# Kernel tuning notes

Measured on AMD Instinct MI355X. Metric: run time of the kernel, lower is better.

The kernel has to match this reference:

```python
import jax, jax.numpy as jnp
import numpy as np
import math

B, T, F_ = 4, 1024, 1024
TO_DIM, FROM_DIM, LATENT, H = 1024, 1024, 1024, 16
HEAD_DIM = LATENT // H

def _linear_params(key, in_dim, out_dim):
    kw, kb = jax.random.split(key)
    bound = 1.0 / math.sqrt(in_dim)
    W = jax.random.uniform(kw, (out_dim, in_dim), minval=-bound, maxval=bound, dtype=jnp.float32)
    b = jax.random.uniform(kb, (out_dim,), minval=-bound, maxval=bound, dtype=jnp.float32)
    return W, b

def setup_inputs() -> dict:
    key = jax.random.key(0)
    ks = jax.random.split(key, 7)
    X_to = jax.random.normal(ks[0], (B, T, TO_DIM), dtype=jnp.float32)
    X_from = jax.random.normal(ks[1], (B, F_, FROM_DIM), dtype=jnp.float32)
    mask_from = jax.random.randint(ks[2], (B, T, F_), 0, 2, dtype=jnp.int32)
    Wq, bq = _linear_params(ks[3], TO_DIM, LATENT)
    Wk, bk = _linear_params(ks[4], FROM_DIM, LATENT)
    Wv, bv = _linear_params(ks[5], FROM_DIM, LATENT)
    Wo, bo = _linear_params(ks[6], LATENT, TO_DIM)
    return {"X_to": X_to, "X_from": X_from, "mask_from": mask_from,
            "Wq": Wq, "bq": bq, "Wk": Wk, "bk": bk, "Wv": Wv, "bv": bv, "Wo": Wo, "bo": bo}

def _split_heads(x):
    # [b, t, (h k)] -> [b, h, t, k]
    b, t, _ = x.shape
    return x.reshape(b, t, H, HEAD_DIM).transpose(0, 2, 1, 3)

def reference(X_to, X_from, mask_from, Wq, bq, Wk, bk, Wv, bv, Wo, bo):
    Q = _split_heads(X_to @ Wq.T + bq)
    # NOTE: source swaps names — K comes from v_linear, V from k_linear. Reproduced literally.
    K = _split_heads(X_from @ Wv.T + bv)
    V = _split_heads(X_from @ Wk.T + bk)
    attn = jnp.einsum('bhtk,bhfk->bhtf', Q, K) / math.sqrt(HEAD_DIM)
    attn = jnp.where(mask_from[:, None, :, :] == 0, jnp.float32(-10000.0), attn)
    attn = jax.nn.softmax(attn, axis=-1)
    out = jnp.einsum('bhtf,bhfk->bhtk', attn, V)  # [b,h,t,k]
    out = out.transpose(0, 2, 1, 3).reshape(X_to.shape[0], X_to.shape[1], LATENT)
    return out @ Wo.T + bo
```

## Files before the change

### kernel.cpp

```cpp
#include <hip/hip_runtime.h>
#include <hip/hip_bf16.h>
#include <math.h>

#define BB 4
#define TT 1024
#define FF 1024
#define DIM 1024
#define NH 16
#define HD 64
#define MROWS (BB * TT)
#define FB (FF / 64)

typedef __attribute__((ext_vector_type(8))) short short8;
typedef __attribute__((ext_vector_type(4))) short short4v;
typedef __attribute__((ext_vector_type(4))) float f32x4;
typedef __hip_bfloat16 bf16;

__device__ __forceinline__ void async_copy16(const void* g, void* l) {
    __builtin_amdgcn_global_load_lds((const __attribute__((address_space(1))) void*)g,
                                     (__attribute__((address_space(3))) void*)l,
                                     16, 0, 0);
}

struct ConvArgs {
    const float* src[6];
    bf16* dst[6];
    int nvec[6];
    int blk_end[6];
    const int* mask;
    unsigned long long* Mb;
};

__global__ __launch_bounds__(256) void convert_pack(ConvArgs a) {
    int bx = blockIdx.x;
    if (bx >= a.blk_end[5]) {
        const int lane = threadIdx.x & 63;
        const int waveId = (bx - a.blk_end[5]) * 4 + (threadIdx.x >> 6);
#pragma unroll
        for (int it = 0; it < 16; ++it) {
            int c = waveId * 16 + it;
            int v = a.mask[(size_t)c * 64 + lane];
            unsigned long long bits = __ballot(v != 0);
            if (lane == 0) a.Mb[c] = bits;
        }
        return;
    }
    int seg = 0;
#pragma unroll
    for (int k = 0; k < 5; ++k) if (bx >= a.blk_end[k]) seg = k + 1;
    int b0 = seg ? a.blk_end[seg - 1] : 0;
    int idx = (bx - b0) * 256 + threadIdx.x;
    if (idx >= a.nvec[seg]) return;
    float4 v = ((const float4*)a.src[seg])[idx];
    union { bf16 t[4]; ushort4 u; } o;
    o.t[0] = __float2bfloat16(v.x);
    o.t[1] = __float2bfloat16(v.y);
    o.t[2] = __float2bfloat16(v.z);
    o.t[3] = __float2bfloat16(v.w);
    *(ushort4*)(a.dst[seg] + 4 * (size_t)idx) = o.u;
}

#define BK 64

struct QkvArgs {
    const bf16* A[3]; const bf16* W[3]; const float* bias[3]; bf16* C[3];
    int N[3]; int biasRow[3];
};

__global__ __launch_bounds__(256) void gemm_qkv(QkvArgs q) {
    __shared__ bf16 smem[128 * 132];
    bf16* As = smem;
    bf16* Bs = smem + 128 * BK;

    const int op = blockIdx.z;
    const bf16* A = q.A[op];
    const bf16* W = q.W[op];
    const float* bias = q.bias[op];
    bf16* C = q.C[op];
    const int N = q.N[op];
    const int brow = q.biasRow[op];

    const int lin = blockIdx.x + 8 * blockIdx.y;
    const int xcd = lin & 7;
    const int t   = lin >> 3;
    int m0, n0;
    if (brow) {
        m0 = (((t & 7) + xcd) & 7) * 128;
        n0 = (xcd * 4 + (t >> 3)) * 128;
    } else {
        m0 = (xcd * 4 + (t >> 3)) * 128;
        n0 = (((t & 7) + xcd) & 7) * 128;
    }

    const int tid  = threadIdx.x;
    const int lane = tid & 63;
    const int wave = tid >> 6;
    const int quad = lane >> 4;
    const int l16  = lane & 15;
    const int wm = wave & 1;
    const int wn = wave >> 1;
    const int wbase = tid & ~63;

    f32x4 acc[4][4] = {};

    for (int k0 = 0; k0 < DIM; k0 += BK) {
#pragma unroll
        for (int j = 0; j < 4; ++j) {
            int slot = j * 256 + tid;
            int r = slot >> 3;
            int g = (slot & 7) ^ (r & 7);
            async_copy16(A + (size_t)(m0 + r) * DIM + k0 + g * 8,
                         As + (size_t)(j * 256 + wbase) * 8);
            async_copy16(W + (size_t)(n0 + r) * DIM + k0 + g * 8,
                         Bs + (size_t)(j * 256 + wbase) * 8);
        }
        __syncthreads();

#pragma unroll
        for (int kk = 0; kk < 2; ++kk) {
            short8 a[4], b[4];
#pragma unroll
            for (int mi = 0; mi < 4; ++mi) {
                int r = wm * 64 + mi * 16 + l16;
                int p = (kk * 4 + quad) ^ (r & 7);
                a[mi] = *(const short8*)(As + r * BK + p * 8);
            }
#pragma unroll
            for (int ni = 0; ni < 4; ++ni) {
                int r = wn * 64 + ni * 16 + l16;
                int p = (kk * 4 + quad) ^ (r & 7);
                b[ni] = *(const short8*)(Bs + r * BK + p * 8);
            }
#pragma unroll
            for (int mi = 0; mi < 4; ++mi)
#pragma unroll
                for (int ni = 0; ni < 4; ++ni)
                    acc[mi][ni] = __builtin_amdgcn_mfma_f32_16x16x32_bf16(
                        a[mi], b[ni], acc[mi][ni], 0, 0, 0);
        }
        __syncthreads();
    }

    bf16* Cs = smem;
#pragma unroll
    for (int ni = 0; ni < 4; ++ni) {
        const int nl = wn * 64 + ni * 16 + l16;
        float bcol = brow ? 0.0f : bias[n0 + nl];
#pragma unroll
        for (int mi = 0; mi < 4; ++mi)
#pragma unroll
            for (int i = 0; i < 4; ++i) {
                const int ml = wm * 64 + mi * 16 + quad * 4 + i;
                float v = acc[mi][ni][i] + (brow ? bias[m0 + ml] : bcol);
                Cs[ml * 132 + nl] = __float2bfloat16(v);
            }
    }
    __syncthreads();
#pragma unroll
    for (int j = 0; j < 8; ++j) {
        int slot = j * 256 + tid;
        int rr = slot >> 4, cc = slot & 15;
        short8 v = *(const short8*)(Cs + rr * 132 + cc * 8);
        *(short8*)(C + (size_t)(m0 + rr) * N + n0 + cc * 8) = v;
    }
}

__global__ __launch_bounds__(256) void gemm_o(
    const bf16* __restrict__ A, const bf16* __restrict__ W,
    const float* __restrict__ bias, float* __restrict__ C)
{
    __shared__ float smemf[128 * 66];
    bf16* As = (bf16*)smemf;
    bf16* Bs = As + 128 * BK;

    const int lin = blockIdx.x + 16 * blockIdx.y;
    const int xcd = lin & 7;
    const int t   = lin >> 3;
    const int m0 = (xcd * 4 + (t >> 4)) * 128;
    const int n0 = (((t & 15) + 2 * xcd) & 15) * 64;

    const int tid  = threadIdx.x;
    const int lane = tid & 63;
    const int wave = tid >> 6;
    const int quad = lane >> 4;
    const int l16  = lane & 15;
    const int wm = wave & 1;
    const int wn = wave >> 1;
    const int wbase = tid & ~63;

    f32x4 acc[4][2] = {};

    for (int k0 = 0; k0 < DIM; k0 += BK) {
#pragma unroll
        for (int j = 0; j < 4; ++j) {
            int slot = j * 256 + tid;
            int r = slot >> 3;
            int g = (slot & 7) ^ (r & 7);
            async_copy16(A + (size_t)(m0 + r) * DIM + k0 + g * 8,
                         As + (size_t)(j * 256 + wbase) * 8);
        }
#pragma unroll
        for (int j = 0; j < 2; ++j) {
            int slot = j * 256 + tid;
            int r = slot >> 3;
            int g = (slot & 7) ^ (r & 7);
            async_copy16(W + (size_t)(n0 + r) * DIM + k0 + g * 8,
                         Bs + (size_t)(j * 256 + wbase) * 8);
        }
        __syncthreads();

#pragma unroll
        for (int kk = 0; kk < 2; ++kk) {
            short8 a[4], b[2];
#pragma unroll
            for (int mi = 0; mi < 4; ++mi) {
                int r = wm * 64 + mi * 16 + l16;
                int p = (kk * 4 + quad) ^ (r & 7);
                a[mi] = *(const short8*)(As + r * BK + p * 8);
            }
#pragma unroll
            for (int ni = 0; ni < 2; ++ni) {
                int r = wn * 32 + ni * 16 + l16;
                int p = (kk * 4 + quad) ^ (r & 7);
                b[ni] = *(const short8*)(Bs + r * BK + p * 8);
            }
#pragma unroll
            for (int mi = 0; mi < 4; ++mi)
#pragma unroll
                for (int ni = 0; ni < 2; ++ni)
                    acc[mi][ni] = __builtin_amdgcn_mfma_f32_16x16x32_bf16(
                        a[mi], b[ni], acc[mi][ni], 0, 0, 0);
        }
        __syncthreads();
    }

    float* Cs = smemf;
#pragma unroll
    for (int ni = 0; ni < 2; ++ni) {
        const int nl = wn * 32 + ni * 16 + l16;
        const float bcol = bias[n0 + nl];
#pragma unroll
        for (int mi = 0; mi < 4; ++mi)
#pragma unroll
            for (int i = 0; i < 4; ++i) {
                const int ml = wm * 64 + mi * 16 + quad * 4 + i;
                Cs[ml * 66 + nl] = acc[mi][ni][i] + bcol;
            }
    }
    __syncthreads();
#pragma unroll
    for (int j = 0; j < 8; ++j) {
        int slot = j * 256 + tid;
        int rr = slot >> 4, cc = slot & 15;
        float4 v = *(const float4*)(Cs + rr * 66 + cc * 4);
        *(float4*)(C + (size_t)(m0 + rr) * DIM + n0 + cc * 4) = v;
    }
}

__global__ __launch_bounds__(256, 4) void attn_kernel(
    const bf16* Qg, const bf16* __restrict__ Kg, const bf16* __restrict__ Vtg,
    const unsigned long long* __restrict__ Mbits, bf16* Og)
{
    __shared__ bf16 Ks[128 * 64];
    __shared__ bf16 Vts[64 * 128];
    __shared__ bf16 Pt[64 * 136];
    __shared__ float ls[64];

    const int tid  = threadIdx.x;
    const int lane = tid & 63;
    const int wave = tid >> 6;
    const int quad = lane >> 4;
    const int l16  = lane & 15;

    const int lin = blockIdx.x + 16 * (blockIdx.y + 16 * blockIdx.z);
    const int xcd = lin & 7;
    const int t   = lin >> 3;
    const int bh  = xcd * 8 + (t >> 4);
    const int b   = bh >> 4;
    const int h   = bh & 15;
    const int t0  = (t & 15) * 64;

    const size_t qrow0 = (size_t)b * TT + t0;
    const size_t krow0 = (size_t)b * FF;
    const int wbase = tid & ~63;
    const int myrow = wave * 16 + l16;

    const bf16* qptr = Qg + (qrow0 + myrow) * DIM + h * HD;
    short8 qb0 = *(const short8*)(qptr + quad * 8);
    short8 qb1 = *(const short8*)(qptr + 32 + quad * 8);

    const unsigned long long* mrow = Mbits + (qrow0 + myrow) * FB;
    unsigned long long w0 = mrow[0];
    unsigned long long w1 = mrow[1];

    float lsum = 0.f;
    f32x4 oacc[4] = {};

#pragma unroll 1
    for (int it = 0; it < 8; ++it) {
        const int f0 = it * 128;
#pragma unroll
        for (int j = 0; j < 4; ++j) {
            int slot = j * 256 + tid;
            int rk = slot >> 3;
            int gk = (slot & 7) ^ (rk & 7);
            async_copy16(Kg + (krow0 + f0 + rk) * DIM + h * HD + gk * 8,
                         Ks + (size_t)(j * 256 + wbase) * 8);
            int rv = slot >> 4;
            int gv = (slot & 15) ^ (rv & 15);
            async_copy16(Vtg + (size_t)(h * HD + rv) * MROWS + b * FF + f0 + gv * 8,
                         Vts + (size_t)(j * 256 + wbase) * 8);
        }
        unsigned long long nw0 = 0, nw1 = 0;
        if (it < 7) { nw0 = mrow[2 * it + 2]; nw1 = mrow[2 * it + 3]; }
        __syncthreads();

        f32x4 sacc[8];
#pragma unroll
        for (int ft = 0; ft < 8; ++ft) {
            int r = ft * 16 + l16;
            short8 ka0 = *(const short8*)(Ks + r * 64 + ((quad       ^ (r & 7)) * 8));
            short8 ka1 = *(const short8*)(Ks + r * 64 + (((quad + 4) ^ (r & 7)) * 8));
            f32x4 s = {};
            s = __builtin_amdgcn_mfma_f32_16x16x32_bf16(ka0, qb0, s, 0, 0, 0);
            s = __builtin_amdgcn_mfma_f32_16x16x32_bf16(ka1, qb1, s, 0, 0, 0);
            sacc[ft] = s;
        }

#pragma unroll
        for (int ft = 0; ft < 8; ++ft) {
            const unsigned long long word = (ft < 4) ? w0 : w1;
            const unsigned bits4 =
                (unsigned)(word >> ((ft & 3) * 16 + quad * 4)) & 0xFu;
            union { short4v v; short s[4]; } pk;
            float psum = 0.f;
#pragma unroll
            for (int i = 0; i < 4; ++i) {
                float p = (bits4 >> i) & 1u ? __expf(sacc[ft][i] * 0.125f) : 0.f;
                psum += p;
                pk.s[i] = (short)__bfloat16_as_ushort(__float2bfloat16(p));
            }
            lsum += psum;
            *(short4v*)(Pt + myrow * 136 + ft * 16 + quad * 4) = pk.v;
        }
        w0 = nw0; w1 = nw1;

        short8 pa[4];
#pragma unroll
        for (int kf = 0; kf < 4; ++kf)
            pa[kf] = *(const short8*)(Pt + myrow * 136 + kf * 32 + quad * 8);
#pragma unroll
        for (int nt = 0; nt < 4; ++nt) {
            int rd = nt * 16 + l16;
#pragma unroll
            for (int kf = 0; kf < 4; ++kf) {
                int g = (kf * 4 + quad) ^ (rd & 15);
                short8 vb = *(const short8*)(Vts + rd * 128 + g * 8);
                oacc[nt] = __builtin_amdgcn_mfma_f32_16x16x32_bf16(pa[kf], vb, oacc[nt], 0, 0, 0);
            }
        }
        __syncthreads();
    }

    lsum += __shfl_xor(lsum, 16);
    lsum += __shfl_xor(lsum, 32);
    if (quad == 0) ls[myrow] = lsum;

#pragma unroll
    for (int i = 0; i < 4; ++i) {
        float inv = 1.0f / ls[wave * 16 + quad * 4 + i];
        const int prow = wave * 16 + quad * 4 + i;
#pragma unroll
        for (int nt = 0; nt < 4; ++nt)
            Pt[prow * 136 + nt * 16 + l16] = __float2bfloat16(oacc[nt][i] * inv);
    }
    __syncthreads();
#pragma unroll
    for (int j = 0; j < 2; ++j) {
        int s = j * 256 + tid;
        int rr = s >> 3, off = (s & 7) * 8;
        short8 v = *(const short8*)(Pt + rr * 136 + off);
        *(short8*)(Og + (qrow0 + rr) * DIM + h * HD + off) = v;
    }
}

extern "C" void kernel_launch(void* const* d_in, const int* in_sizes, int n_in,
                              void* d_out, int out_size, void* d_ws, size_t ws_size,
                              hipStream_t stream) {
    const float* X_to   = (const float*)d_in[0];
    const float* X_from = (const float*)d_in[1];
    const int*   mask   = (const int*)  d_in[2];
    const float* Wq     = (const float*)d_in[3];
    const float* bq     = (const float*)d_in[4];
    const float* Wk     = (const float*)d_in[5];
    const float* bk     = (const float*)d_in[6];
    const float* Wv     = (const float*)d_in[7];
    const float* bv     = (const float*)d_in[8];
    const float* Wo     = (const float*)d_in[9];
    const float* bo     = (const float*)d_in[10];
    float* out = (float*)d_out;

    char* ws = (char*)d_ws;
    bf16* Xt16 = (bf16*)(ws);
    bf16* Xf16 = (bf16*)(ws + (8u  << 20));
    bf16* Wq16 = (bf16*)(ws + (16u << 20));
    bf16* Wv16 = (bf16*)(ws + (18u << 20));
    bf16* Wk16 = (bf16*)(ws + (20u << 20));
    bf16* Wo16 = (bf16*)(ws + (22u << 20));
    bf16* Q16  = (bf16*)(ws + (24u << 20));
    bf16* K16  = (bf16*)(ws + (32u << 20));
    bf16* Vt16 = (bf16*)(ws + (40u << 20));
    unsigned long long* Mb = (unsigned long long*)(ws + (48u << 20));

    ConvArgs ca;
    ca.src[0] = X_to;   ca.dst[0] = Xt16; ca.nvec[0] = MROWS * DIM / 4;
    ca.src[1] = X_from; ca.dst[1] = Xf16; ca.nvec[1] = MROWS * DIM / 4;
    ca.src[2] = Wq;     ca.dst[2] = Wq16; ca.nvec[2] = DIM * DIM / 4;
    ca.src[3] = Wv;     ca.dst[3] = Wv16; ca.nvec[3] = DIM * DIM / 4;
    ca.src[4] = Wk;     ca.dst[4] = Wk16; ca.nvec[4] = DIM * DIM / 4;
    ca.src[5] = Wo;     ca.dst[5] = Wo16; ca.nvec[5] = DIM * DIM / 4;
    int cum = 0;
    for (int k = 0; k < 6; ++k) { cum += ca.nvec[k] / 256; ca.blk_end[k] = cum; }
    ca.mask = mask; ca.Mb = Mb;
    convert_pack<<<cum + 1024, 256, 0, stream>>>(ca);

    QkvArgs qa;
    qa.A[0] = Xt16; qa.W[0] = Wq16; qa.bias[0] = bq; qa.C[0] = Q16;
    qa.N[0] = DIM; qa.biasRow[0] = 0;
    qa.A[1] = Xf16; qa.W[1] = Wv16; qa.bias[1] = bv; qa.C[1] = K16;
    qa.N[1] = DIM; qa.biasRow[1] = 0;
    qa.A[2] = Wk16; qa.W[2] = Xf16; qa.bias[2] = bk; qa.C[2] = Vt16;
    qa.N[2] = MROWS; qa.biasRow[2] = 1;
    gemm_qkv<<<dim3(8, 32, 3), 256, 0, stream>>>(qa);

    attn_kernel<<<dim3(TT / 64, NH, BB), 256, 0, stream>>>(
        Q16, K16, Vt16, Mb, Q16);

    gemm_o<<<dim3(DIM / 64, MROWS / 128), 256, 0, stream>>>(Q16, Wo16, bo, out);
}
```

Baseline: 229.9 us.

## Rewrite QKV GEMM as 256x256-tile, 8-wave double-buffered pipelined kernel

The QKV projection GEMM moves from 128x128 tiles with 4 waves and a synchronous load-then-compute loop to 256x256 tiles with 8 waves. It uses double-buffered LDS with async global-to-LDS copies staged one and two k-steps ahead, explicit vmcnt waits and barriers, and setprio around MFMA phases. This is meant to hide global load latency behind MFMA work and raise arithmetic intensity per tile. The grid shrinks to 192 blocks, which underfills the machine's CUs. The much larger LDS footprint also limits occupancy.

```diff
diff --git a/kernel.cpp b/kernel.cpp
--- a/kernel.cpp
+++ b/kernel.cpp
@@ -67,12 +67,14 @@
     int N[3]; int biasRow[3];
 };
 
-__global__ __launch_bounds__(256) void gemm_qkv(QkvArgs q) {
-    __shared__ bf16 smem[128 * 132];
-    bf16* As = smem;
-    bf16* Bs = smem + 128 * BK;
-
-    const int op = blockIdx.z;
+#define BARRIER() asm volatile("s_barrier" ::: "memory")
+#define WAITVM4() asm volatile("s_waitcnt vmcnt(4)" ::: "memory")
+#define WAITVM0() asm volatile("s_waitcnt vmcnt(0)" ::: "memory")
+
+__global__ __launch_bounds__(512) void gemm_qkv(QkvArgs q) {
+    __shared__ bf16 lds[67584];
+
+    const int op = blockIdx.y;
     const bf16* A = q.A[op];
     const bf16* W = q.W[op];
     const float* bias = q.bias[op];
@@ -80,89 +82,129 @@
     const int N = q.N[op];
     const int brow = q.biasRow[op];
 
-    const int lin = blockIdx.x + 8 * blockIdx.y;
+    const int lin = blockIdx.x;
     const int xcd = lin & 7;
-    const int t   = lin >> 3;
-    int m0, n0;
-    if (brow) {
-        m0 = (((t & 7) + xcd) & 7) * 128;
-        n0 = (xcd * 4 + (t >> 3)) * 128;
-    } else {
-        m0 = (xcd * 4 + (t >> 3)) * 128;
-        n0 = (((t & 7) + xcd) & 7) * 128;
-    }
+    const int t8  = lin >> 3;
+    int mt, nt;
+    if (brow) { mt = t8 & 3; nt = xcd * 2 + (t8 >> 2); }
+    else      { mt = xcd * 2 + (t8 >> 2); nt = t8 & 3; }
+    const int m0 = mt * 256, n0 = nt * 256;
 
     const int tid  = threadIdx.x;
     const int lane = tid & 63;
     const int wave = tid >> 6;
     const int quad = lane >> 4;
     const int l16  = lane & 15;
-    const int wm = wave & 1;
-    const int wn = wave >> 1;
+    const int wm   = wave >> 2;
+    const int wn   = wave & 3;
     const int wbase = tid & ~63;
 
-    f32x4 acc[4][4] = {};
-
-    for (int k0 = 0; k0 < DIM; k0 += BK) {
-#pragma unroll
-        for (int j = 0; j < 4; ++j) {
-            int slot = j * 256 + tid;
-            int r = slot >> 3;
-            int g = (slot & 7) ^ (r & 7);
-            async_copy16(A + (size_t)(m0 + r) * DIM + k0 + g * 8,
-                         As + (size_t)(j * 256 + wbase) * 8);
-            async_copy16(W + (size_t)(n0 + r) * DIM + k0 + g * 8,
-                         Bs + (size_t)(j * 256 + wbase) * 8);
-        }
-        __syncthreads();
-
-#pragma unroll
-        for (int kk = 0; kk < 2; ++kk) {
-            short8 a[4], b[4];
-#pragma unroll
-            for (int mi = 0; mi < 4; ++mi) {
-                int r = wm * 64 + mi * 16 + l16;
-                int p = (kk * 4 + quad) ^ (r & 7);
-                a[mi] = *(const short8*)(As + r * BK + p * 8);
-            }
-#pragma unroll
-            for (int ni = 0; ni < 4; ++ni) {
-                int r = wn * 64 + ni * 16 + l16;
-                int p = (kk * 4 + quad) ^ (r & 7);
-                b[ni] = *(const short8*)(Bs + r * BK + p * 8);
-            }
-#pragma unroll
-            for (int mi = 0; mi < 4; ++mi)
-#pragma unroll
-                for (int ni = 0; ni < 4; ++ni)
-                    acc[mi][ni] = __builtin_amdgcn_mfma_f32_16x16x32_bf16(
-                        a[mi], b[ni], acc[mi][ni], 0, 0, 0);
-        }
-        __syncthreads();
-    }
-
-    bf16* Cs = smem;
+    const int srow = tid >> 3;
+    const int scol = (tid & 7) ^ (srow & 7);
+    const bf16* pA = A + (size_t)(m0 + srow) * DIM + scol * 8;
+    const bf16* pB = W + (size_t)(n0 + srow) * DIM + scol * 8;
+
+#define STAGE(P, ISB, TTL, HH) do { \
+    const bf16* s_ = (P) + (size_t)(HH) * (128 * DIM) + (TTL) * 64; \
+    bf16* d_ = lds + ((TTL) & 1) * 32768 + (ISB) * 16384 + (HH) * 8192 + wbase * 8; \
+    async_copy16(s_, d_); \
+    async_copy16(s_ + 64 * DIM, d_ + 4096); \
+} while (0)
+
+    f32x4 acc[8][4] = {};
+    short8 a[4][2], b[4][2];
+
+    STAGE(pA, 0, 0, 0); STAGE(pB, 1, 0, 0);
+    STAGE(pA, 0, 0, 1); STAGE(pB, 1, 0, 1);
+    STAGE(pA, 0, 1, 0); STAGE(pB, 1, 1, 0);
+    WAITVM4();
+    BARRIER();
+
+#define LDA(AH) do { \
+    _Pragma("unroll") for (int miq = 0; miq < 4; ++miq) { \
+        int r_ = wm * 128 + ((AH) * 4 + miq) * 16 + l16; \
+        const bf16* ba_ = Ab + r_ * 64; \
+        a[miq][0] = *(const short8*)(ba_ + ((quad ^ (r_ & 7)) * 8)); \
+        a[miq][1] = *(const short8*)(ba_ + (((quad + 4) ^ (r_ & 7)) * 8)); \
+    } } while (0)
+
+#define LDB(BH) do { \
+    _Pragma("unroll") for (int niq = 0; niq < 2; ++niq) { \
+        int r_ = wn * 64 + ((BH) * 2 + niq) * 16 + l16; \
+        const bf16* bb_ = Bb + r_ * 64; \
+        b[(BH) * 2 + niq][0] = *(const short8*)(bb_ + ((quad ^ (r_ & 7)) * 8)); \
+        b[(BH) * 2 + niq][1] = *(const short8*)(bb_ + (((quad + 4) ^ (r_ & 7)) * 8)); \
+    } } while (0)
+
+#define MMA(AH, BH) do { \
+    _Pragma("unroll") for (int miq = 0; miq < 4; ++miq) \
+    _Pragma("unroll") for (int niq = 0; niq < 2; ++niq) { \
+        f32x4& c_ = acc[(AH) * 4 + miq][(BH) * 2 + niq]; \
+        c_ = __builtin_amdgcn_mfma_f32_16x16x32_bf16(a[miq][0], b[(BH) * 2 + niq][0], c_, 0, 0, 0); \
+        c_ = __builtin_amdgcn_mfma_f32_16x16x32_bf16(a[miq][1], b[(BH) * 2 + niq][1], c_, 0, 0, 0); \
+    } } while (0)
+
+#define PHASE_MFMA(AH, BH) do { \
+    BARRIER(); __builtin_amdgcn_sched_barrier(0); \
+    __builtin_amdgcn_s_setprio(1); \
+    MMA(AH, BH); \
+    __builtin_amdgcn_s_setprio(0); \
+    __builtin_amdgcn_sched_barrier(0); \
+} while (0)
+
+#pragma unroll 2
+    for (int t = 0; t < 16; ++t) {
+        const bf16* Ab = lds + (t & 1) * 32768;
+        const bf16* Bb = Ab + 16384;
+
+        LDA(0); LDB(0);
+        if (t + 1 < 16) STAGE(pA, 0, t + 1, 1);
+        PHASE_MFMA(0, 0);
+        BARRIER();
+
+        LDB(1);
+        if (t + 1 < 16) STAGE(pB, 1, t + 1, 1);
+        PHASE_MFMA(0, 1);
+        BARRIER();
+
+        LDA(1);
+        if (t + 2 < 16) STAGE(pA, 0, t + 2, 0);
+        PHASE_MFMA(1, 0);
+        BARRIER();
+
+        if (t + 2 < 16) STAGE(pB, 1, t + 2, 0);
+        PHASE_MFMA(1, 1);
+        if (t < 14) { WAITVM4(); } else if (t == 14) { WAITVM0(); }
+        BARRIER();
+    }
+
+    bf16* Cs = lds;
 #pragma unroll
     for (int ni = 0; ni < 4; ++ni) {
         const int nl = wn * 64 + ni * 16 + l16;
         float bcol = brow ? 0.0f : bias[n0 + nl];
 #pragma unroll
-        for (int mi = 0; mi < 4; ++mi)
+        for (int mi = 0; mi < 8; ++mi)
 #pragma unroll
             for (int i = 0; i < 4; ++i) {
-                const int ml = wm * 64 + mi * 16 + quad * 4 + i;
+                const int ml = wm * 128 + mi * 16 + quad * 4 + i;
                 float v = acc[mi][ni][i] + (brow ? bias[m0 + ml] : bcol);
-                Cs[ml * 132 + nl] = __float2bfloat16(v);
+                Cs[ml * 264 + nl] = __float2bfloat16(v);
             }
     }
     __syncthreads();
 #pragma unroll
-    for (int j = 0; j < 8; ++j) {
-        int slot = j * 256 + tid;
-        int rr = slot >> 4, cc = slot & 15;
-        short8 v = *(const short8*)(Cs + rr * 132 + cc * 8);
+    for (int j = 0; j < 16; ++j) {
+        int slot = j * 512 + tid;
+        int rr = slot >> 5, cc = slot & 31;
+        short8 v = *(const short8*)(Cs + rr * 264 + cc * 8);
         *(short8*)(C + (size_t)(m0 + rr) * N + n0 + cc * 8) = v;
     }
+#undef STAGE
+#undef LDA
+#undef LDB
+#undef MMA
+#undef PHASE_MFMA
 }
 
 __global__ __launch_bounds__(256) void gemm_o(
@@ -431,7 +473,7 @@
     qa.N[1] = DIM; qa.biasRow[1] = 0;
     qa.A[2] = Wk16; qa.W[2] = Xf16; qa.bias[2] = bk; qa.C[2] = Vt16;
     qa.N[2] = MROWS; qa.biasRow[2] = 1;
-    gemm_qkv<<<dim3(8, 32, 3), 256, 0, stream>>>(qa);
+    gemm_qkv<<<dim3(64, 3), 512, 0, stream>>>(qa);
 
     attn_kernel<<<dim3(TT / 64, NH, BB), 256, 0, stream>>>(
         Q16, K16, Vt16, Mb, Q16);
```

After: 223.8 us. 1.03x faster.
